# Performance work log

Hardware: AMD Instinct MI355X
Metric: run time of the kernel (lower is better)

The kernel has to match this reference:

```python
import jax, jax.numpy as jnp
import numpy as np

B, N, D = 8, 8192, 512
HID_ATT = D // 8          # input_dim // num_heads = 64
TOPK = max(1, int(N * 0.3))  # 2457


def _mlp2(x, W1, b1, W2, b2):
    # 2-layer MLP: Linear -> GELU -> Linear (inference mode: dropout/norm off)
    h = jax.nn.gelu(x @ W1 + b1)
    return h @ W2 + b2


def setup_inputs() -> dict:
    key = jax.random.key(0)
    ks = jax.random.split(key, 9)
    s = lambda k, sh, fan: jax.random.normal(k, sh, jnp.float32) * (1.0 / np.sqrt(fan))
    return {
        "x": jax.random.normal(ks[0], (B, N, D), jnp.float32),
        # attention-score MLP: D -> HID_ATT -> 1
        "aW1": s(ks[1], (D, HID_ATT), D),
        "ab1": jnp.zeros((HID_ATT,), jnp.float32),
        "aW2": s(ks[2], (HID_ATT, 1), HID_ATT),
        "ab2": jnp.zeros((1,), jnp.float32),
        # projection MLP: D -> D -> D
        "pW1": s(ks[3], (D, D), D),
        "pb1": jnp.zeros((D,), jnp.float32),
        "pW2": s(ks[4], (D, D), D),
        "pb2": jnp.zeros((D,), jnp.float32),
    }


def reference(x, aW1, ab1, aW2, ab2, pW1, pb1, pW2, pb2):
    # per-instance attention score -> sigmoid weight, [B, N]
    weights = jax.nn.sigmoid(_mlp2(x, aW1, ab1, aW2, ab2)[..., 0])
    # top-k per bag (largest)
    topk_scores, topk_idx = jax.lax.top_k(weights, TOPK)  # [B, TOPK]
    # gather selected instances, scale by score, mean over selected -> [B, D]
    sel = jnp.take_along_axis(x, topk_idx[..., None], axis=1)  # [B, TOPK, D]
    emb = jnp.mean(sel * topk_scores[..., None], axis=1)       # [B, D]
    projection = _mlp2(emb, pW1, pb1, pW2, pb2)                # [B, D]
    return projection, weights
```

## Files before the change

kernel.cpp:

```cpp
#include <hip/hip_runtime.h>
#include <math.h>

#define B_BAGS 8
#define N_INST 8192
#define D_DIM  512
#define H_ATT  64
#define TOPK_K 2457
#define ROWS_TOTAL (B_BAGS * N_INST)

typedef __attribute__((ext_vector_type(8))) short bf16x8;
typedef __attribute__((ext_vector_type(4))) float f32x4;

#define WS_W1T_HI 0
#define WS_W1T_LO 65536
#define WS_META   131072
#define WS_PART3  131584
#define WS_PART1  (WS_PART3 + 8*64*512*4)
#define WS_PART2  (WS_PART1 + 8*8*512*4)

__device__ __forceinline__ unsigned short bf16_rn(float f) {
  unsigned int x = __float_as_uint(f);
  unsigned int r = (x + 0x7FFFu + ((x >> 16) & 1u)) >> 16;
  return (unsigned short)r;
}
__device__ __forceinline__ float bf16_f(unsigned short u) {
  return __uint_as_float(((unsigned int)u) << 16);
}
__device__ __forceinline__ float gelu_f(float v) {
  float u = 0.7978845608028654f * (v + 0.044715f * v * v * v);
  return 0.5f * v * (1.0f + tanhf(u));
}

__device__ __forceinline__ void cvt_hilo(const float4 u, const float4 v,
                                         bf16x8& h, bf16x8& l) {
  float f[8] = {u.x, u.y, u.z, u.w, v.x, v.y, v.z, v.w};
#pragma unroll
  for (int i = 0; i < 8; i++) {
    unsigned int b = __float_as_uint(f[i]);
    unsigned int hb = b & 0xFFFF0000u;
    float r = f[i] - __uint_as_float(hb);
    h[i] = (short)(b >> 16);
    l[i] = (short)(__float_as_uint(r) >> 16);
  }
}

__global__ __launch_bounds__(256) void k_prep(const float* __restrict__ aW1,
                                              unsigned short* __restrict__ hi,
                                              unsigned short* __restrict__ lo) {
  int o = blockIdx.x * 256 + threadIdx.x;
  if (o >= H_ATT * D_DIM) return;
  int n = o >> 9;
  int k = o & 511;
  float v = aW1[k * H_ATT + n];
  unsigned short h = bf16_rn(v);
  unsigned short l = bf16_rn(v - bf16_f(h));
  hi[o] = h;
  lo[o] = l;
}

#define BM 128

__global__ __launch_bounds__(256) void k_scores(
    const float* __restrict__ x,
    const unsigned short* __restrict__ w1t_hi,
    const unsigned short* __restrict__ w1t_lo,
    const float* __restrict__ ab1, const float* __restrict__ aW2,
    const float* __restrict__ ab2, float* __restrict__ wout) {
  int tid = threadIdx.x;
  int wave = tid >> 6, lane = tid & 63;
  int c0 = lane & 15, quad = lane >> 4;
  int rowBase = blockIdx.x * BM;

  const float* xr[2];
  xr[0] = x + (size_t)(rowBase + wave * 32 + c0) * D_DIM;
  xr[1] = xr[0] + 16 * D_DIM;
  const int kq = quad * 8;

  f32x4 acc[2][4];
#pragma unroll
  for (int s = 0; s < 2; s++)
#pragma unroll
    for (int t = 0; t < 4; t++) acc[s][t] = (f32x4){0.f, 0.f, 0.f, 0.f};

  const unsigned short* bh0 = w1t_hi + c0 * D_DIM + kq;
  const unsigned short* bl0 = w1t_lo + c0 * D_DIM + kq;

  float4 a0[2], a1[2], n0[2], n1[2];
#pragma unroll
  for (int s = 0; s < 2; s++) {
    a0[s] = *reinterpret_cast<const float4*>(xr[s] + kq);
    a1[s] = *reinterpret_cast<const float4*>(xr[s] + kq + 4);
  }

  for (int ks = 0; ks < 16; ks++) {
    if (ks < 15) {
      int kb = (ks + 1) * 32 + kq;
#pragma unroll
      for (int s = 0; s < 2; s++) {
        n0[s] = *reinterpret_cast<const float4*>(xr[s] + kb);
        n1[s] = *reinterpret_cast<const float4*>(xr[s] + kb + 4);
      }
    }
    bf16x8 bfh[4], bfl[4];
#pragma unroll
    for (int t = 0; t < 4; t++) {
      bfh[t] = *reinterpret_cast<const bf16x8*>(bh0 + t * 16 * D_DIM + ks * 32);
      bfl[t] = *reinterpret_cast<const bf16x8*>(bl0 + t * 16 * D_DIM + ks * 32);
    }
    bf16x8 afh[2], afl[2];
#pragma unroll
    for (int s = 0; s < 2; s++) cvt_hilo(a0[s], a1[s], afh[s], afl[s]);
#pragma unroll
    for (int s = 0; s < 2; s++)
#pragma unroll
      for (int t = 0; t < 4; t++) {
        acc[s][t] = __builtin_amdgcn_mfma_f32_16x16x32_bf16(afl[s], bfh[t], acc[s][t], 0, 0, 0);
        acc[s][t] = __builtin_amdgcn_mfma_f32_16x16x32_bf16(afh[s], bfl[t], acc[s][t], 0, 0, 0);
        acc[s][t] = __builtin_amdgcn_mfma_f32_16x16x32_bf16(afh[s], bfh[t], acc[s][t], 0, 0, 0);
      }
#pragma unroll
    for (int s = 0; s < 2; s++) { a0[s] = n0[s]; a1[s] = n1[s]; }
  }

  float w2v[4], b1v[4];
#pragma unroll
  for (int t = 0; t < 4; t++) {
    w2v[t] = aW2[t * 16 + c0];
    b1v[t] = ab1[t * 16 + c0];
  }
  float bias2 = ab2[0];
#pragma unroll
  for (int s = 0; s < 2; s++) {
    float p[4] = {0.f, 0.f, 0.f, 0.f};
#pragma unroll
    for (int t = 0; t < 4; t++)
#pragma unroll
      for (int r = 0; r < 4; r++) {
        float h = gelu_f(acc[s][t][r] + b1v[t]);
        p[r] += h * w2v[t];
      }
#pragma unroll
    for (int off = 1; off < 16; off <<= 1)
#pragma unroll
      for (int r = 0; r < 4; r++) p[r] += __shfl_xor(p[r], off, 64);
    if (c0 == 0) {
      int row = rowBase + wave * 32 + s * 16 + quad * 4;
#pragma unroll
      for (int r = 0; r < 4; r++) {
        float sc = p[r] + bias2;
        wout[row + r] = 1.0f / (1.0f + expf(-sc));
      }
    }
  }
}

__global__ __launch_bounds__(256) void k_topk(const float* __restrict__ wout,
                                              unsigned int* __restrict__ meta) {
  int b = blockIdx.x;
  const float* w = wout + b * N_INST;
  int tid = threadIdx.x;
  unsigned int v[32];
#pragma unroll
  for (int j = 0; j < 32; j++) v[j] = __float_as_uint(w[j * 256 + tid]);

  __shared__ int red[2][4];
  int lane = tid & 63, wv = tid >> 6;
  int pb = 0;

  auto blocksum = [&](int c) -> int {
#pragma unroll
    for (int off = 32; off > 0; off >>= 1) c += __shfl_down(c, off, 64);
    if (lane == 0) red[pb][wv] = c;
    __syncthreads();
    int s = red[pb][0] + red[pb][1] + red[pb][2] + red[pb][3];
    pb ^= 1;
    return s;
  };

  unsigned int lo = 0u, hi = 0x3F800001u;
  while (hi - lo > 1u) {
    unsigned int mid = lo + ((hi - lo) >> 1);
    int c = 0;
#pragma unroll
    for (int j = 0; j < 32; j++) c += (v[j] >= mid) ? 1 : 0;
    int s = blocksum(c);
    if (s >= TOPK_K) lo = mid; else hi = mid;
  }
  unsigned int T = lo;

  int c1;
  {
    int c = 0;
#pragma unroll
    for (int j = 0; j < 32; j++) c += (v[j] > T) ? 1 : 0;
    c1 = blocksum(c);
  }
  int needed = TOPK_K - c1;

  unsigned int tm = 0;
#pragma unroll
  for (int j = 0; j < 32; j++) tm |= (v[j] == T ? 1u : 0u) << j;
  int lom = -1, him = N_INST - 1;
  while (him - lom > 1) {
    int mid = (lom + him) >> 1;
    unsigned int mask = 0u;
    if (mid >= tid) {
      unsigned int jmax = (unsigned int)(mid - tid) >> 8;
      mask = (2u << jmax) - 1u;
    }
    int s = blocksum((int)__popc(tm & mask));
    if (s >= needed) him = mid; else lom = mid;
  }
  if (tid == 0) {
    meta[b] = T;
    ((int*)meta)[8 + b] = him;
  }
}

__global__ __launch_bounds__(256) void k_gather(const float* __restrict__ x,
                                                const float* __restrict__ wout,
                                                const unsigned int* __restrict__ meta,
                                                float* __restrict__ part3) {
  int b = blockIdx.x >> 6;
  int blk = blockIdx.x & 63;
  unsigned int T = meta[b];
  int Icut = ((const int*)meta)[8 + b];
  int tid = threadIdx.x;

  __shared__ int idxs[128];
  __shared__ float wgts[128];
  __shared__ int wcnt[2];

  int r = blk * 128 + tid;
  bool sel = false;
  float wvv = 0.f;
  int pos = 0;
  if (tid < 128) {
    wvv = wout[b * N_INST + r];
    unsigned int wu = __float_as_uint(wvv);
    sel = (wu > T) || (wu == T && r <= Icut);
    unsigned long long m = __ballot(sel);
    int lane = tid & 63;
    pos = __popcll(m & ((1ull << lane) - 1ull));
    if (lane == 0) wcnt[tid >> 6] = __popcll(m);
  }
  __syncthreads();
  int total = wcnt[0] + wcnt[1];
  if (sel) {
    int base = (tid >= 64) ? wcnt[0] : 0;
    idxs[base + pos] = r;
    wgts[base + pos] = wvv;
  }
  __syncthreads();

  float2 acc = {0.f, 0.f};
  const float* xb = x + (size_t)b * N_INST * D_DIM;
#pragma unroll 8
  for (int i = 0; i < total; i++) {
    int rr = idxs[i];
    float ww = wgts[i];
    const float2 xv = *reinterpret_cast<const float2*>(xb + (size_t)rr * D_DIM + tid * 2);
    acc.x += ww * xv.x;
    acc.y += ww * xv.y;
  }
  *reinterpret_cast<float2*>(part3 + (size_t)(b * 64 + blk) * D_DIM + tid * 2) = acc;
}

__global__ __launch_bounds__(256) void k_proj1(const float* __restrict__ part3,
                                               const float* __restrict__ pW1,
                                               float* __restrict__ part1) {
  int jt = blockIdx.x & 7, kt = blockIdx.x >> 3;
  __shared__ float emb_s[512];
  int tid = threadIdx.x;
#pragma unroll
  for (int h = 0; h < 2; h++) {
    int vi = tid + h * 256;
    int b = vi >> 6, d0 = vi & 63;
    const float* p = part3 + (size_t)b * 64 * 512 + kt * 64 + d0;
    float e = 0.f;
#pragma unroll 8
    for (int j = 0; j < 64; j++) e += p[j * 512];
    emb_s[vi] = e * (1.0f / TOPK_K);
  }
  __syncthreads();
  int col = tid & 63, bg = tid >> 6;
  float a0 = 0.f, a1 = 0.f;
  const float* wrow = pW1 + (size_t)(kt * 64) * 512 + jt * 64 + col;
#pragma unroll 8
  for (int q = 0; q < 64; q++) {
    float wq = wrow[q * 512];
    a0 += emb_s[(bg * 2) * 64 + q] * wq;
    a1 += emb_s[(bg * 2 + 1) * 64 + q] * wq;
  }
  part1[kt * 4096 + (bg * 2) * 512 + jt * 64 + col] = a0;
  part1[kt * 4096 + (bg * 2 + 1) * 512 + jt * 64 + col] = a1;
}

__global__ __launch_bounds__(256) void k_proj2(const float* __restrict__ part1,
                                               const float* __restrict__ pb1,
                                               const float* __restrict__ pW2,
                                               float* __restrict__ part2) {
  int jt = blockIdx.x & 7, kt = blockIdx.x >> 3;
  __shared__ float h_s[512];
  int tid = threadIdx.x;
#pragma unroll
  for (int h = 0; h < 2; h++) {
    int vi = tid + h * 256;
    int b = vi >> 6, j0 = vi & 63;
    int jj = kt * 64 + j0;
    float s = pb1[jj];
#pragma unroll
    for (int p = 0; p < 8; p++) s += part1[p * 4096 + b * 512 + jj];
    h_s[vi] = gelu_f(s);
  }
  __syncthreads();
  int col = tid & 63, bg = tid >> 6;
  float a0 = 0.f, a1 = 0.f;
  const float* wrow = pW2 + (size_t)(kt * 64) * 512 + jt * 64 + col;
#pragma unroll 8
  for (int q = 0; q < 64; q++) {
    float wq = wrow[q * 512];
    a0 += h_s[(bg * 2) * 64 + q] * wq;
    a1 += h_s[(bg * 2 + 1) * 64 + q] * wq;
  }
  part2[kt * 4096 + (bg * 2) * 512 + jt * 64 + col] = a0;
  part2[kt * 4096 + (bg * 2 + 1) * 512 + jt * 64 + col] = a1;
}

__global__ __launch_bounds__(512) void k_proj3(const float* __restrict__ part2,
                                               const float* __restrict__ pb2,
                                               float* __restrict__ out) {
  int o = blockIdx.x * 512 + threadIdx.x;
  int bj = o & 511;
  float s = pb2[bj];
#pragma unroll
  for (int p = 0; p < 8; p++) s += part2[p * 4096 + o];
  out[o] = s;
}

extern "C" void kernel_launch(void* const* d_in, const int* in_sizes, int n_in,
                              void* d_out, int out_size, void* d_ws, size_t ws_size,
                              hipStream_t stream) {
  (void)in_sizes; (void)n_in; (void)out_size; (void)ws_size;
  const float* x   = (const float*)d_in[0];
  const float* aW1 = (const float*)d_in[1];
  const float* ab1 = (const float*)d_in[2];
  const float* aW2 = (const float*)d_in[3];
  const float* ab2 = (const float*)d_in[4];
  const float* pW1 = (const float*)d_in[5];
  const float* pb1 = (const float*)d_in[6];
  const float* pW2 = (const float*)d_in[7];
  const float* pb2 = (const float*)d_in[8];

  float* out  = (float*)d_out;
  float* wout = out + B_BAGS * D_DIM;

  char* ws = (char*)d_ws;
  unsigned short* w1t_hi = (unsigned short*)(ws + WS_W1T_HI);
  unsigned short* w1t_lo = (unsigned short*)(ws + WS_W1T_LO);
  unsigned int*   meta   = (unsigned int*)(ws + WS_META);
  float* part3 = (float*)(ws + WS_PART3);
  float* part1 = (float*)(ws + WS_PART1);
  float* part2 = (float*)(ws + WS_PART2);

  k_prep<<<dim3((H_ATT * D_DIM + 255) / 256), dim3(256), 0, stream>>>(aW1, w1t_hi, w1t_lo);
  k_scores<<<dim3(ROWS_TOTAL / BM), dim3(256), 0, stream>>>(x, w1t_hi, w1t_lo, ab1, aW2, ab2, wout);
  k_topk<<<dim3(B_BAGS), dim3(256), 0, stream>>>(wout, meta);
  k_gather<<<dim3(B_BAGS * 64), dim3(256), 0, stream>>>(x, wout, meta, part3);
  k_proj1<<<dim3(64), dim3(256), 0, stream>>>(part3, pW1, part1);
  k_proj2<<<dim3(64), dim3(256), 0, stream>>>(part1, pb1, pW2, part2);
  k_proj3<<<dim3(B_BAGS), dim3(512), 0, stream>>>(part2, pb2, out);
}
```

Before: 273.4 us.

## Shrink score tile to 64 rows with B prefetch; gather rows as float4 split across halves

New measurement: 293.2 us. +7.2%, slower.

```diff
diff --git a/kernel.cpp b/kernel.cpp
--- a/kernel.cpp
+++ b/kernel.cpp
@@ -58,7 +58,7 @@
   lo[o] = l;
 }
 
-#define BM 128
+#define BM 64
 
 __global__ __launch_bounds__(256) void k_scores(
     const float* __restrict__ x,
@@ -69,57 +69,50 @@
   int tid = threadIdx.x;
   int wave = tid >> 6, lane = tid & 63;
   int c0 = lane & 15, quad = lane >> 4;
-  int rowBase = blockIdx.x * BM;
-
-  const float* xr[2];
-  xr[0] = x + (size_t)(rowBase + wave * 32 + c0) * D_DIM;
-  xr[1] = xr[0] + 16 * D_DIM;
+  int rowBase = blockIdx.x * BM + wave * 16;
   const int kq = quad * 8;
 
-  f32x4 acc[2][4];
-#pragma unroll
-  for (int s = 0; s < 2; s++)
-#pragma unroll
-    for (int t = 0; t < 4; t++) acc[s][t] = (f32x4){0.f, 0.f, 0.f, 0.f};
-
+  const float* xr = x + (size_t)(rowBase + c0) * D_DIM;
   const unsigned short* bh0 = w1t_hi + c0 * D_DIM + kq;
   const unsigned short* bl0 = w1t_lo + c0 * D_DIM + kq;
 
-  float4 a0[2], a1[2], n0[2], n1[2];
-#pragma unroll
-  for (int s = 0; s < 2; s++) {
-    a0[s] = *reinterpret_cast<const float4*>(xr[s] + kq);
-    a1[s] = *reinterpret_cast<const float4*>(xr[s] + kq + 4);
+  f32x4 acc[4];
+#pragma unroll
+  for (int t = 0; t < 4; t++) acc[t] = (f32x4){0.f, 0.f, 0.f, 0.f};
+
+  float4 a0, a1, na0, na1;
+  bf16x8 bfh[4], bfl[4], nbh[4], nbl[4];
+
+  a0 = *reinterpret_cast<const float4*>(xr + kq);
+  a1 = *reinterpret_cast<const float4*>(xr + kq + 4);
+#pragma unroll
+  for (int t = 0; t < 4; t++) {
+    bfh[t] = *reinterpret_cast<const bf16x8*>(bh0 + t * 16 * D_DIM);
+    bfl[t] = *reinterpret_cast<const bf16x8*>(bl0 + t * 16 * D_DIM);
   }
 
   for (int ks = 0; ks < 16; ks++) {
     if (ks < 15) {
-      int kb = (ks + 1) * 32 + kq;
-#pragma unroll
-      for (int s = 0; s < 2; s++) {
-        n0[s] = *reinterpret_cast<const float4*>(xr[s] + kb);
-        n1[s] = *reinterpret_cast<const float4*>(xr[s] + kb + 4);
+      int kb = (ks + 1) * 32;
+      na0 = *reinterpret_cast<const float4*>(xr + kb + kq);
+      na1 = *reinterpret_cast<const float4*>(xr + kb + kq + 4);
+#pragma unroll
+      for (int t = 0; t < 4; t++) {
+        nbh[t] = *reinterpret_cast<const bf16x8*>(bh0 + t * 16 * D_DIM + kb);
+        nbl[t] = *reinterpret_cast<const bf16x8*>(bl0 + t * 16 * D_DIM + kb);
       }
     }
-    bf16x8 bfh[4], bfl[4];
+    bf16x8 afh, afl;
+    cvt_hilo(a0, a1, afh, afl);
 #pragma unroll
     for (int t = 0; t < 4; t++) {
-      bfh[t] = *reinterpret_cast<const bf16x8*>(bh0 + t * 16 * D_DIM + ks * 32);
-      bfl[t] = *reinterpret_cast<const bf16x8*>(bl0 + t * 16 * D_DIM + ks * 32);
-    }
-    bf16x8 afh[2], afl[2];
-#pragma unroll
-    for (int s = 0; s < 2; s++) cvt_hilo(a0[s], a1[s], afh[s], afl[s]);
-#pragma unroll
-    for (int s = 0; s < 2; s++)
-#pragma unroll
-      for (int t = 0; t < 4; t++) {
-        acc[s][t] = __builtin_amdgcn_mfma_f32_16x16x32_bf16(afl[s], bfh[t], acc[s][t], 0, 0, 0);
-        acc[s][t] = __builtin_amdgcn_mfma_f32_16x16x32_bf16(afh[s], bfl[t], acc[s][t], 0, 0, 0);
-        acc[s][t] = __builtin_amdgcn_mfma_f32_16x16x32_bf16(afh[s], bfh[t], acc[s][t], 0, 0, 0);
-      }
-#pragma unroll
-    for (int s = 0; s < 2; s++) { a0[s] = n0[s]; a1[s] = n1[s]; }
+      acc[t] = __builtin_amdgcn_mfma_f32_16x16x32_bf16(afl, bfh[t], acc[t], 0, 0, 0);
+      acc[t] = __builtin_amdgcn_mfma_f32_16x16x32_bf16(afh, bfl[t], acc[t], 0, 0, 0);
+      acc[t] = __builtin_amdgcn_mfma_f32_16x16x32_bf16(afh, bfh[t], acc[t], 0, 0, 0);
+    }
+    a0 = na0; a1 = na1;
+#pragma unroll
+    for (int t = 0; t < 4; t++) { bfh[t] = nbh[t]; bfl[t] = nbl[t]; }
   }
 
   float w2v[4], b1v[4];
@@ -129,27 +122,24 @@
     b1v[t] = ab1[t * 16 + c0];
   }
   float bias2 = ab2[0];
-#pragma unroll
-  for (int s = 0; s < 2; s++) {
-    float p[4] = {0.f, 0.f, 0.f, 0.f};
-#pragma unroll
-    for (int t = 0; t < 4; t++)
-#pragma unroll
-      for (int r = 0; r < 4; r++) {
-        float h = gelu_f(acc[s][t][r] + b1v[t]);
-        p[r] += h * w2v[t];
-      }
-#pragma unroll
-    for (int off = 1; off < 16; off <<= 1)
-#pragma unroll
-      for (int r = 0; r < 4; r++) p[r] += __shfl_xor(p[r], off, 64);
-    if (c0 == 0) {
-      int row = rowBase + wave * 32 + s * 16 + quad * 4;
-#pragma unroll
-      for (int r = 0; r < 4; r++) {
-        float sc = p[r] + bias2;
-        wout[row + r] = 1.0f / (1.0f + expf(-sc));
-      }
+  float p[4] = {0.f, 0.f, 0.f, 0.f};
+#pragma unroll
+  for (int t = 0; t < 4; t++)
+#pragma unroll
+    for (int r = 0; r < 4; r++) {
+      float h = gelu_f(acc[t][r] + b1v[t]);
+      p[r] += h * w2v[t];
+    }
+#pragma unroll
+  for (int off = 1; off < 16; off <<= 1)
+#pragma unroll
+    for (int r = 0; r < 4; r++) p[r] += __shfl_xor(p[r], off, 64);
+  if (c0 == 0) {
+    int row = rowBase + quad * 4;
+#pragma unroll
+    for (int r = 0; r < 4; r++) {
+      float sc = p[r] + bias2;
+      wout[row + r] = 1.0f / (1.0f + expf(-sc));
     }
   }
 }
@@ -230,6 +220,7 @@
   __shared__ int idxs[128];
   __shared__ float wgts[128];
   __shared__ int wcnt[2];
+  __shared__ float4 xfer[128];
 
   int r = blk * 128 + tid;
   bool sel = false;
@@ -253,17 +244,31 @@
   }
   __syncthreads();
 
-  float2 acc = {0.f, 0.f};
+  int half = tid >> 7;
+  int L = tid & 127;
+  float4 acc = {0.f, 0.f, 0.f, 0.f};
   const float* xb = x + (size_t)b * N_INST * D_DIM;
-#pragma unroll 8
-  for (int i = 0; i < total; i++) {
-    int rr = idxs[i];
-    float ww = wgts[i];
-    const float2 xv = *reinterpret_cast<const float2*>(xb + (size_t)rr * D_DIM + tid * 2);
-    acc.x += ww * xv.x;
-    acc.y += ww * xv.y;
-  }
-  *reinterpret_cast<float2*>(part3 + (size_t)(b * 64 + blk) * D_DIM + tid * 2) = acc;
+  int i2 = total & ~1;
+#pragma unroll 4
+  for (int i = 0; i < i2; i += 2) {
+    int rr = idxs[i + half];
+    float ww = wgts[i + half];
+    const float4 xv = *reinterpret_cast<const float4*>(xb + (size_t)rr * D_DIM + L * 4);
+    acc.x += ww * xv.x; acc.y += ww * xv.y; acc.z += ww * xv.z; acc.w += ww * xv.w;
+  }
+  if ((total & 1) && half == 0) {
+    int rr = idxs[i2];
+    float ww = wgts[i2];
+    const float4 xv = *reinterpret_cast<const float4*>(xb + (size_t)rr * D_DIM + L * 4);
+    acc.x += ww * xv.x; acc.y += ww * xv.y; acc.z += ww * xv.z; acc.w += ww * xv.w;
+  }
+  if (half == 1) xfer[L] = acc;
+  __syncthreads();
+  if (half == 0) {
+    float4 o = xfer[L];
+    acc.x += o.x; acc.y += o.y; acc.z += o.z; acc.w += o.w;
+    *reinterpret_cast<float4*>(part3 + (size_t)(b * 64 + blk) * D_DIM + L * 4) = acc;
+  }
 }
 
 __global__ __launch_bounds__(256) void k_proj1(const float* __restrict__ part3,
```
